# Kernel optimization log

Hardware: AMD Instinct MI355X
Metric: run time of the kernel (lower is better)

Reference implementation:

```python
import jax, jax.numpy as jnp
import numpy as np

N_NODES = 100000
N_EDGES = 1600000
D = 64


def setup_inputs() -> dict:
    key = jax.random.key(0)
    k1, k2, k3, k4 = jax.random.split(key, 4)
    x = jax.random.normal(k1, (N_NODES, D), dtype=jnp.float32)
    edge_index = jax.random.randint(k2, (2, N_EDGES), 0, N_NODES, dtype=jnp.int64)
    edge_attr = jax.random.normal(k3, (N_EDGES, D), dtype=jnp.float32)
    eps = jnp.zeros((1,), dtype=jnp.float32)
    W = jax.random.normal(k4, (D, D), dtype=jnp.float32) * (1.0 / np.sqrt(D))
    b = jnp.zeros((D,), dtype=jnp.float32)
    return {"x": x, "edge_index": edge_index, "edge_attr": edge_attr,
            "eps": eps, "W": W, "b": b}


def reference(x, edge_index, edge_attr, eps, W, b):
    # GIN branch with agg='point', point_encoder='RELU', use_linear=True
    dst, src = edge_index[0], edge_index[1]
    self_element = x * (1.0 + eps[0])                       # [N, D]
    message = jax.nn.relu(x[src] + edge_attr)               # [E, D]
    x_agg = jax.ops.segment_sum(message, dst, num_segments=x.shape[0])  # [N, D]
    h = self_element + x_agg
    return h @ W + b                                        # Linear(d, d_output)
```

## Files before the change

### kernel.cpp

```cpp
#include <hip/hip_runtime.h>

typedef float f4 __attribute__((ext_vector_type(4)));

constexpr int NN = 100000;
constexpr int NE = 1600000;
constexpr int SCAN_BLK = 1024;
constexpr int NB = (NN + SCAN_BLK - 1) / SCAN_BLK;

__device__ __forceinline__ f4 relu_add(f4 a, f4 b) {
    f4 s = a + b;
    s.x = fmaxf(s.x, 0.f);
    s.y = fmaxf(s.y, 0.f);
    s.z = fmaxf(s.z, 0.f);
    s.w = fmaxf(s.w, 0.f);
    return s;
}

__device__ __forceinline__ f4 bf16x4_to_f4(uint2 u) {
    f4 r;
    r.x = __uint_as_float((u.x & 0xFFFFu) << 16);
    r.y = __uint_as_float(u.x & 0xFFFF0000u);
    r.z = __uint_as_float((u.y & 0xFFFFu) << 16);
    r.w = __uint_as_float(u.y & 0xFFFF0000u);
    return r;
}

__device__ __forceinline__ unsigned f2bf(float f) {
    unsigned u = __float_as_uint(f);
    return (u + 0x7FFFu + ((u >> 16) & 1u)) >> 16;
}

__device__ __forceinline__ unsigned pack2bf(float lo, float hi) {
    return f2bf(lo) | (f2bf(hi) << 16);
}


__global__ __launch_bounds__(256) void k_init(const float* __restrict__ x,
                                              const float* __restrict__ eps,
                                              float* __restrict__ out) {
    const float s = 1.0f + eps[0];
    const float4* x4 = (const float4*)x;
    float4* o4 = (float4*)out;
    const int total = NN * 16;
    for (int i = blockIdx.x * blockDim.x + threadIdx.x; i < total;
         i += gridDim.x * blockDim.x) {
        float4 v = x4[i];
        v.x *= s; v.y *= s; v.z *= s; v.w *= s;
        o4[i] = v;
    }
}

__global__ __launch_bounds__(256) void k_edges(const float* __restrict__ x,
                                               const int* __restrict__ ei,
                                               const float* __restrict__ ea,
                                               float* __restrict__ out) {
    const int* dst = ei;
    const int* src = ei + NE;
    const float4* ea4 = (const float4*)ea;
    const float4* x4 = (const float4*)x;
    const int total = NE * 16;
    for (int g = blockIdx.x * blockDim.x + threadIdx.x; g < total;
         g += gridDim.x * blockDim.x) {
        const int e = g >> 4;
        const int c = g & 15;
        const int s = src[e];
        const int d = dst[e];
        float4 a  = ea4[g];
        float4 xv = x4[s * 16 + c];
        float* base = out + d * 64 + c * 4;
        atomicAdd(base + 0, fmaxf(xv.x + a.x, 0.0f));
        atomicAdd(base + 1, fmaxf(xv.y + a.y, 0.0f));
        atomicAdd(base + 2, fmaxf(xv.z + a.z, 0.0f));
        atomicAdd(base + 3, fmaxf(xv.w + a.w, 0.0f));
    }
}

__global__ __launch_bounds__(256) void k_linear2(const float* __restrict__ W,
                                                 const float* __restrict__ bias,
                                                 float* __restrict__ out) {
    __shared__ float Ws[64 * 64];
    __shared__ float bs[64];
    for (int i = threadIdx.x; i < 1024; i += 256)
        ((float4*)Ws)[i] = ((const float4*)W)[i];
    if (threadIdx.x < 16)
        ((float4*)bs)[threadIdx.x] = ((const float4*)bias)[threadIdx.x];
    __syncthreads();

    const int l16 = threadIdx.x & 15;
    const int gid = (blockIdx.x * 256 + threadIdx.x) >> 4;
    const float4* Ws4 = (const float4*)Ws;
    float4* out4 = (float4*)out;

    const float4 h4 = out4[gid * 16 + l16];
    float4 o = ((const float4*)bs)[l16];
#pragma unroll
    for (int d = 0; d < 64; ++d) {
        const int q = d >> 2;
        const int r = d & 3;
        float hd;
        if (r == 0)      hd = __shfl(h4.x, q, 16);
        else if (r == 1) hd = __shfl(h4.y, q, 16);
        else if (r == 2) hd = __shfl(h4.z, q, 16);
        else             hd = __shfl(h4.w, q, 16);
        const float4 w = Ws4[d * 16 + l16];
        o.x = fmaf(hd, w.x, o.x);
        o.y = fmaf(hd, w.y, o.y);
        o.z = fmaf(hd, w.z, o.z);
        o.w = fmaf(hd, w.w, o.w);
    }
    out4[gid * 16 + l16] = o;
}


__global__ __launch_bounds__(256) void k_hist(const int* __restrict__ dst,
                                              int* __restrict__ counts) {
    const int4* d4 = (const int4*)dst;
    const int total = NE / 4;
    for (int i = blockIdx.x * blockDim.x + threadIdx.x; i < total;
         i += gridDim.x * blockDim.x) {
        const int4 d = d4[i];
        atomicAdd(&counts[d.x], 1);
        atomicAdd(&counts[d.y], 1);
        atomicAdd(&counts[d.z], 1);
        atomicAdd(&counts[d.w], 1);
    }
}

__global__ __launch_bounds__(256) void k_scan_block(const int* __restrict__ counts,
                                                    int* __restrict__ offsets,
                                                    int* __restrict__ bsum) {
    __shared__ int sd[256];
    const int t = threadIdx.x;
    const int base = blockIdx.x * SCAN_BLK;
    int c[4];
    int s = 0;
#pragma unroll
    for (int k = 0; k < 4; ++k) {
        const int i = base + t * 4 + k;
        c[k] = (i < NN) ? counts[i] : 0;
        s += c[k];
    }
    sd[t] = s;
    __syncthreads();
#pragma unroll
    for (int off = 1; off < 256; off <<= 1) {
        int v = (t >= off) ? sd[t - off] : 0;
        __syncthreads();
        sd[t] += v;
        __syncthreads();
    }
    int excl = sd[t] - s;
#pragma unroll
    for (int k = 0; k < 4; ++k) {
        const int i = base + t * 4 + k;
        if (i < NN) offsets[i] = excl;
        excl += c[k];
    }
    if (t == 255) bsum[blockIdx.x] = sd[255];
}

__global__ __launch_bounds__(256) void k_scan_finish(int* __restrict__ offsets,
                                                     const int* __restrict__ bsum,
                                                     int* __restrict__ cursor) {
    __shared__ int sd[128];
    const int t = threadIdx.x;
    if (t < 128) {
        const int v = (t < NB) ? bsum[t] : 0;
        sd[t] = v;
    }
    __syncthreads();
#pragma unroll
    for (int off = 1; off < 128; off <<= 1) {
        int u = 0;
        if (t < 128 && t >= off) u = sd[t - off];
        __syncthreads();
        if (t < 128) sd[t] += u;
        __syncthreads();
    }
    for (int i = blockIdx.x * blockDim.x + t; i < NN;
         i += gridDim.x * blockDim.x) {
        const int b = i >> 10;
        const int v = offsets[i] + sd[b] - bsum[b];
        offsets[i] = v;
        cursor[i] = v;
    }
    if (blockIdx.x == 0 && t == 0) offsets[NN] = NE;
}

__global__ __launch_bounds__(256) void k_scatter_val(const float* __restrict__ x,
                                                     const int* __restrict__ ei,
                                                     const float* __restrict__ ea,
                                                     int* __restrict__ cursor,
                                                     unsigned short* __restrict__ vals) {
    const int* dst = ei;
    const int* src = ei + NE;
    const int l16 = threadIdx.x & 15;
    const int gid0 = (blockIdx.x * blockDim.x + threadIdx.x) >> 4;
    const int ngrp = (gridDim.x * blockDim.x) >> 4;
    const f4* x4 = (const f4*)x;
    const f4* ea4 = (const f4*)ea;
    uint2* v2 = (uint2*)vals;

    for (int e = gid0; e < NE; e += ngrp) {
        const int d = dst[e];
        const int s = src[e];
        int pos = 0;
        if (l16 == 0) pos = atomicAdd(&cursor[d], 1);
        pos = __shfl(pos, 0, 16);
        const f4 A = ea4[e * 16 + l16];
        const f4 X = x4[s * 16 + l16];
        const f4 m = relu_add(X, A);
        uint2 o;
        o.x = pack2bf(m.x, m.y);
        o.y = pack2bf(m.z, m.w);
        v2[(size_t)pos * 16 + l16] = o;
    }
}

__global__ __launch_bounds__(256) void k_segsum_lin(const float* __restrict__ x,
                                                    const unsigned short* __restrict__ vals,
                                                    const int* __restrict__ offsets,
                                                    const float* __restrict__ epsp,
                                                    const float* __restrict__ W,
                                                    const float* __restrict__ bias,
                                                    float* __restrict__ out) {
    __shared__ float Ws[64 * 64];
    __shared__ float bs[64];
    for (int i = threadIdx.x; i < 1024; i += 256)
        ((float4*)Ws)[i] = ((const float4*)W)[i];
    if (threadIdx.x < 16)
        ((float4*)bs)[threadIdx.x] = ((const float4*)bias)[threadIdx.x];
    __syncthreads();

    const float epsv = 1.0f + epsp[0];
    const int l16 = threadIdx.x & 15;
    const int n = (blockIdx.x * 256 + threadIdx.x) >> 4;
    const f4* x4 = (const f4*)x;
    const uint2* v2 = (const uint2*)vals;
    const f4* Ws4 = (const f4*)Ws;
    f4* out4 = (f4*)out;

    const int beg = offsets[n];
    const int end = offsets[n + 1];
    f4 acc = {0.f, 0.f, 0.f, 0.f};

    int j = beg;
    for (; j + 4 <= end; j += 4) {
        const uint2 u0 = v2[(size_t)(j + 0) * 16 + l16];
        const uint2 u1 = v2[(size_t)(j + 1) * 16 + l16];
        const uint2 u2 = v2[(size_t)(j + 2) * 16 + l16];
        const uint2 u3 = v2[(size_t)(j + 3) * 16 + l16];
        acc += bf16x4_to_f4(u0) + bf16x4_to_f4(u1) +
               bf16x4_to_f4(u2) + bf16x4_to_f4(u3);
    }
    for (; j < end; ++j)
        acc += bf16x4_to_f4(v2[(size_t)j * 16 + l16]);

    const f4 xs = x4[n * 16 + l16];
    f4 h;
    h.x = fmaf(xs.x, epsv, acc.x);
    h.y = fmaf(xs.y, epsv, acc.y);
    h.z = fmaf(xs.z, epsv, acc.z);
    h.w = fmaf(xs.w, epsv, acc.w);

    f4 o = ((const f4*)bs)[l16];
#pragma unroll
    for (int d = 0; d < 64; ++d) {
        const int q = d >> 2;
        const int r = d & 3;
        float hd;
        if (r == 0)      hd = __shfl(h.x, q, 16);
        else if (r == 1) hd = __shfl(h.y, q, 16);
        else if (r == 2) hd = __shfl(h.z, q, 16);
        else             hd = __shfl(h.w, q, 16);
        const f4 w = Ws4[d * 16 + l16];
        o.x = fmaf(hd, w.x, o.x);
        o.y = fmaf(hd, w.y, o.y);
        o.z = fmaf(hd, w.z, o.z);
        o.w = fmaf(hd, w.w, o.w);
    }
    out4[n * 16 + l16] = o;
}

extern "C" void kernel_launch(void* const* d_in, const int* in_sizes, int n_in,
                              void* d_out, int out_size, void* d_ws, size_t ws_size,
                              hipStream_t stream) {
    const float* x   = (const float*)d_in[0];
    const int*   ei  = (const int*)d_in[1];
    const float* ea  = (const float*)d_in[2];
    const float* eps = (const float*)d_in[3];
    const float* W   = (const float*)d_in[4];
    const float* b   = (const float*)d_in[5];
    float* out = (float*)d_out;

    const int* dst = ei;

    unsigned short* vals = (unsigned short*)d_ws;
    int* counts  = (int*)(vals + (size_t)NE * 64);
    int* offsets = counts + NN;
    int* cursor  = offsets + NN + 1;
    int* bsum    = cursor + NN;
    const size_t ws_needed = (size_t)NE * 128 +
                             (size_t)(3 * NN + 1 + 128) * sizeof(int);

    if (ws_size < ws_needed) {
        k_init<<<2048, 256, 0, stream>>>(x, eps, out);
        k_edges<<<2048, 256, 0, stream>>>(x, ei, ea, out);
        k_linear2<<<NN * 16 / 256, 256, 0, stream>>>(W, b, out);
        return;
    }

    (void)hipMemsetAsync(counts, 0, (size_t)NN * sizeof(int), stream);
    k_hist<<<1024, 256, 0, stream>>>(dst, counts);
    k_scan_block<<<NB, 256, 0, stream>>>(counts, offsets, bsum);
    k_scan_finish<<<256, 256, 0, stream>>>(offsets, bsum, cursor);
    k_scatter_val<<<4096, 256, 0, stream>>>(x, ei, ea, cursor, vals);
    k_segsum_lin<<<NN * 16 / 256, 256, 0, stream>>>(x, vals, offsets, eps,
                                                    W, b, out);
}
```

Measured before the change: 313.4 us.

## Record per-edge rank in histogram pass to remove atomics from scatter

The histogram kernel now keeps the value returned by each atomicAdd as a per-edge rank and stores it in a new workspace array. The scatter kernel then computes each edge's CSR slot as offsets[dst] + rank, so it no longer needs a second round of atomics on a cursor array. The scatter loop also handles two edges per 16-lane group to put more independent gathers in flight. The cost is an extra 6.4 MB rank array that is written in the histogram pass and read back during the scatter.

Measured after the change: 296.9 us. 5.3% less time.

```diff
diff --git a/kernel.cpp b/kernel.cpp
--- a/kernel.cpp
+++ b/kernel.cpp
@@ -112,17 +112,21 @@
 }
 
 
-__global__ __launch_bounds__(256) void k_hist(const int* __restrict__ dst,
-                                              int* __restrict__ counts) {
+__global__ __launch_bounds__(256) void k_rank(const int* __restrict__ dst,
+                                              int* __restrict__ cursor,
+                                              int* __restrict__ rank) {
     const int4* d4 = (const int4*)dst;
+    int4* r4 = (int4*)rank;
     const int total = NE / 4;
     for (int i = blockIdx.x * blockDim.x + threadIdx.x; i < total;
          i += gridDim.x * blockDim.x) {
         const int4 d = d4[i];
-        atomicAdd(&counts[d.x], 1);
-        atomicAdd(&counts[d.y], 1);
-        atomicAdd(&counts[d.z], 1);
-        atomicAdd(&counts[d.w], 1);
+        int4 r;
+        r.x = atomicAdd(&cursor[d.x], 1);
+        r.y = atomicAdd(&cursor[d.y], 1);
+        r.z = atomicAdd(&cursor[d.z], 1);
+        r.w = atomicAdd(&cursor[d.w], 1);
+        r4[i] = r;
     }
 }
 
@@ -160,8 +164,7 @@
 }
 
 __global__ __launch_bounds__(256) void k_scan_finish(int* __restrict__ offsets,
-                                                     const int* __restrict__ bsum,
-                                                     int* __restrict__ cursor) {
+                                                     const int* __restrict__ bsum) {
     __shared__ int sd[128];
     const int t = threadIdx.x;
     if (t < 128) {
@@ -180,9 +183,7 @@
     for (int i = blockIdx.x * blockDim.x + t; i < NN;
          i += gridDim.x * blockDim.x) {
         const int b = i >> 10;
-        const int v = offsets[i] + sd[b] - bsum[b];
-        offsets[i] = v;
-        cursor[i] = v;
+        offsets[i] += sd[b] - bsum[b];
     }
     if (blockIdx.x == 0 && t == 0) offsets[NN] = NE;
 }
@@ -190,7 +191,8 @@
 __global__ __launch_bounds__(256) void k_scatter_val(const float* __restrict__ x,
                                                      const int* __restrict__ ei,
                                                      const float* __restrict__ ea,
-                                                     int* __restrict__ cursor,
+                                                     const int* __restrict__ offsets,
+                                                     const int* __restrict__ rank,
                                                      unsigned short* __restrict__ vals) {
     const int* dst = ei;
     const int* src = ei + NE;
@@ -201,19 +203,27 @@
     const f4* ea4 = (const f4*)ea;
     uint2* v2 = (uint2*)vals;
 
-    for (int e = gid0; e < NE; e += ngrp) {
-        const int d = dst[e];
-        const int s = src[e];
-        int pos = 0;
-        if (l16 == 0) pos = atomicAdd(&cursor[d], 1);
-        pos = __shfl(pos, 0, 16);
-        const f4 A = ea4[e * 16 + l16];
-        const f4 X = x4[s * 16 + l16];
-        const f4 m = relu_add(X, A);
-        uint2 o;
-        o.x = pack2bf(m.x, m.y);
-        o.y = pack2bf(m.z, m.w);
-        v2[(size_t)pos * 16 + l16] = o;
+    const int nbatch = NE / 2;
+    for (int bi = gid0; bi < nbatch; bi += ngrp) {
+        const int e0 = 2 * bi;
+        const int e1 = 2 * bi + 1;
+        const int d0 = dst[e0], d1 = dst[e1];
+        const int s0 = src[e0], s1 = src[e1];
+        const int slot0 = offsets[d0] + rank[e0];
+        const int slot1 = offsets[d1] + rank[e1];
+        const f4 A0 = ea4[(size_t)e0 * 16 + l16];
+        const f4 X0 = x4[(size_t)s0 * 16 + l16];
+        const f4 A1 = ea4[(size_t)e1 * 16 + l16];
+        const f4 X1 = x4[(size_t)s1 * 16 + l16];
+        const f4 m0 = relu_add(X0, A0);
+        const f4 m1 = relu_add(X1, A1);
+        uint2 o0, o1;
+        o0.x = pack2bf(m0.x, m0.y);
+        o0.y = pack2bf(m0.z, m0.w);
+        o1.x = pack2bf(m1.x, m1.y);
+        o1.y = pack2bf(m1.z, m1.w);
+        v2[(size_t)slot0 * 16 + l16] = o0;
+        v2[(size_t)slot1 * 16 + l16] = o1;
     }
 }
 
@@ -296,12 +306,12 @@
     const int* dst = ei;
 
     unsigned short* vals = (unsigned short*)d_ws;
-    int* counts  = (int*)(vals + (size_t)NE * 64);
-    int* offsets = counts + NN;
-    int* cursor  = offsets + NN + 1;
-    int* bsum    = cursor + NN;
-    const size_t ws_needed = (size_t)NE * 128 +
-                             (size_t)(3 * NN + 1 + 128) * sizeof(int);
+    int* rank    = (int*)(vals + (size_t)NE * 64);
+    int* cursor  = rank + NE;
+    int* offsets = cursor + NN;
+    int* bsum    = offsets + NN + 1;
+    const size_t ws_needed = (size_t)NE * 128 + (size_t)NE * 4 +
+                             (size_t)(2 * NN + 1 + 128) * sizeof(int);
 
     if (ws_size < ws_needed) {
         k_init<<<2048, 256, 0, stream>>>(x, eps, out);
@@ -310,11 +320,11 @@
         return;
     }
 
-    (void)hipMemsetAsync(counts, 0, (size_t)NN * sizeof(int), stream);
-    k_hist<<<1024, 256, 0, stream>>>(dst, counts);
-    k_scan_block<<<NB, 256, 0, stream>>>(counts, offsets, bsum);
-    k_scan_finish<<<256, 256, 0, stream>>>(offsets, bsum, cursor);
-    k_scatter_val<<<4096, 256, 0, stream>>>(x, ei, ea, cursor, vals);
+    (void)hipMemsetAsync(cursor, 0, (size_t)NN * sizeof(int), stream);
+    k_rank<<<1024, 256, 0, stream>>>(dst, cursor, rank);
+    k_scan_block<<<NB, 256, 0, stream>>>(cursor, offsets, bsum);
+    k_scan_finish<<<256, 256, 0, stream>>>(offsets, bsum);
+    k_scatter_val<<<4096, 256, 0, stream>>>(x, ei, ea, offsets, rank, vals);
     k_segsum_lin<<<NN * 16 / 256, 256, 0, stream>>>(x, vals, offsets, eps,
                                                     W, b, out);
 }
```
